# Optimization experiments

Hardware: AMD Instinct MI355X
Metric: run time of the kernel (lower is better)

The kernel has to match this reference:

```python
import jax, jax.numpy as jnp
import numpy as np

B, N = 1, 512
CS, CZ = 384, 128
H, DQK, DV, PQK, PV = 12, 16, 16, 4, 8
EPS = 1e-8
SW = float(np.sqrt(1.0 / (3 * DQK)))            # scalar_weights
PW = float(np.sqrt(1.0 / (3 * PQK * 9.0 / 2)))  # point_weights
ZW = float(np.sqrt(1.0 / 3))                    # attention_2d_weights


def _lin(key, din, dout):
    return 0.02 * jax.random.normal(key, (din, dout), dtype=jnp.float32), jnp.zeros((dout,), dtype=jnp.float32)


def setup_inputs():
    key = jax.random.key(0)
    ks = jax.random.split(key, 16)
    Wsq, bsq = _lin(ks[0], CS, H * DQK)
    Wsk, bsk = _lin(ks[1], CS, H * DQK)
    Wsv, bsv = _lin(ks[2], CS, H * DV)
    Wsb, bsb = _lin(ks[3], CZ, H)
    Wpq, bpq = _lin(ks[4], CS, H * PQK * 3)
    Wpk, bpk = _lin(ks[5], CS, H * PQK * 3)
    Wpv, bpv = _lin(ks[6], CS, H * PV * 3)
    Wout, bout = _lin(ks[7], H * (DV + PV * 4 + CZ), CS)
    w_attn = 0.5 * jax.random.normal(ks[8], (3,), dtype=jnp.float32)  # attn_linear weight (1,3)
    b_attn = jnp.zeros((), dtype=jnp.float32)
    tpw = jnp.full((H,), float(np.log(np.e - 1.0)), dtype=jnp.float32)  # trainable_point_weight
    s = jax.random.normal(ks[9], (B, N, CS), dtype=jnp.float32)
    z = jax.random.normal(ks[10], (B, N, N, CZ), dtype=jnp.float32)
    rot = jax.random.normal(ks[11], (B, N, 3, 3), dtype=jnp.float32)
    tran = jax.random.normal(ks[12], (B, N, 3), dtype=jnp.float32)
    res_mask = jnp.ones((B, N), dtype=jnp.float32)
    return dict(s=s, z=z, rot=rot, tran=tran, res_mask=res_mask,
                Wsq=Wsq, bsq=bsq, Wsk=Wsk, bsk=bsk, Wsv=Wsv, bsv=bsv,
                Wsb=Wsb, bsb=bsb, Wpq=Wpq, bpq=bpq, Wpk=Wpk, bpk=bpk,
                Wpv=Wpv, bpv=bpv, w_attn=w_attn, b_attn=b_attn, tpw=tpw,
                Wout=Wout, bout=bout)


def _ipa(s, z, rot, tran, res_mask, Wsq, bsq, Wsk, bsk, Wsv, bsv, Wsb, bsb,
         Wpq, bpq, Wpk, bpk, Wpv, bpv, w_attn, b_attn, tpw, Wout, bout):
    b, n, _ = s.shape
    sq = (s @ Wsq + bsq).reshape(b, n, H, DQK)
    sk = (s @ Wsk + bsk).reshape(b, n, H, DQK)
    sv = (s @ Wsv + bsv).reshape(b, n, H, DV)
    sb = z @ Wsb + bsb  # [b, i, j, h] pair bias

    def to_global(W, bias, p):
        t = (s @ W + bias).reshape(b, n, H, p, 3)
        return jnp.einsum('bnxy,bnhpy->bnhpx', rot, t) + tran[:, :, None, None, :]

    pqg = to_global(Wpq, bpq, PQK)
    pkg = to_global(Wpk, bpk, PQK)
    pvg = to_global(Wpv, bpv, PV)

    diff = pqg[:, :, None] - pkg[:, None, :]          # [b, i, j, h, p, 3]
    sdist = jnp.sum(diff * diff, axis=(-1, -2))       # [b, i, j, h]

    attn_point = -0.5 * jax.nn.softplus(tpw) * sdist * PW
    attn_scalar = jnp.einsum('bihd,bjhd->bijh', sq * SW, sk)
    attn_pair = sb * ZW
    # attn_linear(stack([scalar, point, pair], -1)).squeeze(-1)
    logits = attn_scalar * w_attn[0] + attn_point * w_attn[1] + attn_pair * w_attn[2] + b_attn

    mask2d = res_mask[:, :, None] * res_mask[:, None, :]
    logits = jnp.where(mask2d[..., None] == 0, jnp.finfo(logits.dtype).min, logits)
    attn = jax.nn.softmax(logits, axis=2)             # softmax over j

    r_scalar = jnp.einsum('bijh,bjhd->bihd', attn, sv)
    r_pt_g = jnp.einsum('bijh,bjhpc->bihpc', attn, pvg)
    # rotate back to local frame: R^T (x - t)
    r_pt = jnp.einsum('biyx,bihpy->bihpx', rot, r_pt_g - tran[:, :, None, None, :])
    r_norm = jnp.sqrt(jnp.sum(r_pt * r_pt, axis=-1) + EPS)  # [b, i, h, p]
    r_pair = jnp.einsum('bijh,bijc->bihc', attn, z)

    cat = jnp.concatenate([r_scalar, r_pt.reshape(b, n, H, PV * 3), r_norm, r_pair], axis=-1)
    return cat.reshape(b, n, -1) @ Wout + bout


def reference(s, z, rot, tran, res_mask, Wsq, bsq, Wsk, bsk, Wsv, bsv, Wsb, bsb,
              Wpq, bpq, Wpk, bpk, Wpv, bpv, w_attn, b_attn, tpw, Wout, bout):
    return _ipa(s, z, rot, tran, res_mask, Wsq, bsq, Wsk, bsk, Wsv, bsv, Wsb, bsb,
                Wpq, bpq, Wpk, bpk, Wpv, bpv, w_attn, b_attn, tpw, Wout, bout)
```

## Files before the change

kernel.cpp:

```cpp
#include <hip/hip_runtime.h>
#include <hip/hip_bf16.h>
#include <math.h>

#define NN 512
#define CSD 384
#define CZ 128
#define HH 12
#define TMPW 1152
#define CATH 176
#define CATDIM 2112
#define NSPLIT 6
#define KSPL 352

#define SW 0.14433756729740643f
#define PW 0.13608276348795434f
#define ZW 0.57735026918962576f
#define NEG_INF -3.4028234663852886e38f

typedef float f32x4_t __attribute__((ext_vector_type(4)));
typedef short bf16x8_t __attribute__((ext_vector_type(8)));

union BFU { uint4 q; bf16x8_t v; ushort u[8]; };

static __device__ __forceinline__ ushort f2bf(float f) {
    __hip_bfloat16 h = __float2bfloat16(f);
    return *reinterpret_cast<ushort*>(&h);
}
static __device__ __forceinline__ float bf2f(ushort u) {
    unsigned int v = ((unsigned int)u) << 16;
    return __uint_as_float(v);
}

__global__ void proj_gemm_kernel(const float* __restrict__ s,
                                 const float* __restrict__ Wsq, const float* __restrict__ bsq,
                                 const float* __restrict__ Wsk, const float* __restrict__ bsk,
                                 const float* __restrict__ Wsv, const float* __restrict__ bsv,
                                 const float* __restrict__ Wpq, const float* __restrict__ bpq,
                                 const float* __restrict__ Wpk, const float* __restrict__ bpk,
                                 const float* __restrict__ Wpv, const float* __restrict__ bpv,
                                 float* __restrict__ tmp)
{
    int bx = blockIdx.x;
    int n0 = blockIdx.y * 32;
    int f0 = bx * 48;
    const float* W; const float* bb; int dout; int segstart;
    if (bx < 4)       { W = Wsq; bb = bsq; dout = 192; segstart = 0; }
    else if (bx < 8)  { W = Wsk; bb = bsk; dout = 192; segstart = 192; }
    else if (bx < 12) { W = Wsv; bb = bsv; dout = 192; segstart = 384; }
    else if (bx < 15) { W = Wpq; bb = bpq; dout = 144; segstart = 576; }
    else if (bx < 18) { W = Wpk; bb = bpk; dout = 144; segstart = 720; }
    else              { W = Wpv; bb = bpv; dout = 288; segstart = 864; }
    int colbase = f0 - segstart;

    __shared__ float St[32][34];
    __shared__ float Ws[32][49];
    int tid = threadIdx.x;
    int ty = tid >> 4, tx = tid & 15;
    float acc[2][3] = {{0,0,0},{0,0,0}};

    for (int k0 = 0; k0 < CSD; k0 += 32) {
        {
            int r = tid >> 3, c4 = (tid & 7) * 4;
            float4 v = *(const float4*)&s[(size_t)(n0 + r) * CSD + k0 + c4];
            St[c4 + 0][r] = v.x; St[c4 + 1][r] = v.y; St[c4 + 2][r] = v.z; St[c4 + 3][r] = v.w;
        }
        for (int e = tid; e < 1536; e += 256) {
            int r = e / 48, c = e % 48;
            Ws[r][c] = W[(size_t)(k0 + r) * dout + colbase + c];
        }
        __syncthreads();
        #pragma unroll
        for (int k = 0; k < 32; k++) {
            float2 a = *(const float2*)&St[k][ty * 2];
            float b0 = Ws[k][tx * 3], b1 = Ws[k][tx * 3 + 1], b2 = Ws[k][tx * 3 + 2];
            acc[0][0] += a.x * b0; acc[0][1] += a.x * b1; acc[0][2] += a.x * b2;
            acc[1][0] += a.y * b0; acc[1][1] += a.y * b1; acc[1][2] += a.y * b2;
        }
        __syncthreads();
    }
    float bv0 = bb[colbase + tx * 3], bv1 = bb[colbase + tx * 3 + 1], bv2 = bb[colbase + tx * 3 + 2];
    #pragma unroll
    for (int r = 0; r < 2; r++) {
        float* o = tmp + (size_t)(n0 + ty * 2 + r) * TMPW + f0 + tx * 3;
        o[0] = acc[r][0] + bv0; o[1] = acc[r][1] + bv1; o[2] = acc[r][2] + bv2;
    }
}

__global__ void rotate_kernel(const float* __restrict__ rot, const float* __restrict__ tran,
                              float* __restrict__ tmp)
{
    int pid = blockIdx.x * 256 + threadIdx.x;
    int n = pid / 192, q = pid % 192;
    float* p = tmp + (size_t)n * TMPW + 576 + q * 3;
    float v0 = p[0], v1 = p[1], v2 = p[2];
    const float* R = rot + n * 9;
    const float* T = tran + n * 3;
    p[0] = R[0] * v0 + R[1] * v1 + R[2] * v2 + T[0];
    p[1] = R[3] * v0 + R[4] * v1 + R[5] * v2 + T[1];
    p[2] = R[6] * v0 + R[7] * v1 + R[8] * v2 + T[2];
}

__global__ void pairbias_mfma_kernel(const float* __restrict__ z, const float* __restrict__ Wsb,
                                     const float* __restrict__ watt, float* __restrict__ sbz)
{
    int tid = threadIdx.x;
    int w = tid >> 6, lane = tid & 63;
    int l16 = lane & 15, lhi = lane >> 4;
    float A2 = watt[2] * ZW;

    BFU breg[4];
    #pragma unroll
    for (int kk = 0; kk < 4; kk++) {
        #pragma unroll
        for (int e = 0; e < 8; e++) {
            int k = kk * 32 + lhi * 8 + e;
            float v = (l16 < HH) ? Wsb[k * HH + l16] * A2 : 0.f;
            breg[kk].u[e] = f2bf(v);
        }
    }

    #pragma unroll
    for (int t = 0; t < 4; t++) {
        size_t r0 = (size_t)blockIdx.x * 256 + (size_t)(t * 4 + w) * 16;
        const float* zrow = z + (r0 + l16) * CZ;
        f32x4_t acc = {0.f, 0.f, 0.f, 0.f};
        #pragma unroll
        for (int kk = 0; kk < 4; kk++) {
            int k0 = kk * 32 + lhi * 8;
            float4 f0 = *(const float4*)&zrow[k0];
            float4 f1 = *(const float4*)&zrow[k0 + 4];
            BFU a;
            a.u[0] = f2bf(f0.x); a.u[1] = f2bf(f0.y); a.u[2] = f2bf(f0.z); a.u[3] = f2bf(f0.w);
            a.u[4] = f2bf(f1.x); a.u[5] = f2bf(f1.y); a.u[6] = f2bf(f1.z); a.u[7] = f2bf(f1.w);
            acc = __builtin_amdgcn_mfma_f32_16x16x32_bf16(a.v, breg[kk].v, acc, 0, 0, 0);
        }
        if (l16 < HH) {
            #pragma unroll
            for (int r = 0; r < 4; r++)
                sbz[(r0 + lhi * 4 + r) * HH + l16] = acc[r];
        }
    }
}

__global__ void logits_softmax_kernel(const float* __restrict__ sbz, const float* __restrict__ resm,
                                      const float* __restrict__ bsb,
                                      const float* __restrict__ watt, const float* __restrict__ batt,
                                      const float* __restrict__ tpw, const float* __restrict__ tmp,
                                      ushort* __restrict__ attn_bf)
{
    int i = blockIdx.x;
    __shared__ float lt[NN * 17];
    __shared__ float sqs[192];
    __shared__ float pqi[144];
    __shared__ float cpt[12];
    __shared__ float cb[12];
    int tid = threadIdx.x;
    float w0 = watt[0], w1 = watt[1], w2 = watt[2], ba = batt[0];
    float A2 = w2 * ZW;

    for (int k = tid; k < 192; k += 256) sqs[k] = tmp[(size_t)i * TMPW + k] * (SW * w0);
    if (tid < 144) pqi[tid] = tmp[(size_t)i * TMPW + 576 + tid];
    if (tid < 12) {
        cpt[tid] = -0.5f * log1pf(expf(tpw[tid])) * PW * w1;
        cb[tid]  = A2 * bsb[tid] + ba;
    }
    __syncthreads();

    int jg = tid >> 2, hg = tid & 3, h0 = hg * 3;
    float rmi = resm[i];
    const float* sbi = sbz + (size_t)i * NN * HH;

    #pragma unroll
    for (int rr = 0; rr < 8; rr++) {
        int j = jg + 64 * rr;
        float mj = rmi * resm[j];
        const float* sbr = &sbi[(size_t)j * HH + h0];
        float pb[3] = { sbr[0], sbr[1], sbr[2] };
        #pragma unroll
        for (int t = 0; t < 3; t++) {
            int h = h0 + t;
            const float4* skp = (const float4*)(tmp + (size_t)j * TMPW + 192 + h * 16);
            const float4* sqp = (const float4*)&sqs[h * 16];
            float d0 = 0.f;
            #pragma unroll
            for (int q = 0; q < 4; q++) {
                float4 kv = skp[q];
                float4 qv = sqp[q];
                d0 += qv.x * kv.x + qv.y * kv.y + qv.z * kv.z + qv.w * kv.w;
            }
            const float4* pkp = (const float4*)(tmp + (size_t)j * TMPW + 720 + h * 12);
            const float4* pqp = (const float4*)&pqi[h * 12];
            float sd = 0.f;
            #pragma unroll
            for (int q = 0; q < 3; q++) {
                float4 kv = pkp[q];
                float4 qv = pqp[q];
                float a = qv.x - kv.x, bb2 = qv.y - kv.y, cc = qv.z - kv.z, e = qv.w - kv.w;
                sd += a * a + bb2 * bb2 + cc * cc + e * e;
            }
            float lg = cb[h] + pb[t] + d0 + cpt[h] * sd;
            if (mj == 0.f) lg = NEG_INF;
            lt[j * 17 + h] = lg;
        }
    }
    __syncthreads();

    int wid = tid >> 6, lane = tid & 63;
    #pragma unroll
    for (int t = 0; t < 3; t++) {
        int h = wid * 3 + t;
        float v[8]; float m = -INFINITY;
        #pragma unroll
        for (int u = 0; u < 8; u++) { v[u] = lt[(lane + 64 * u) * 17 + h]; m = fmaxf(m, v[u]); }
        for (int off = 32; off; off >>= 1) m = fmaxf(m, __shfl_xor(m, off));
        float ssum = 0.f;
        #pragma unroll
        for (int u = 0; u < 8; u++) { v[u] = __expf(v[u] - m); ssum += v[u]; }
        for (int off = 32; off; off >>= 1) ssum += __shfl_xor(ssum, off);
        float inv = 1.f / ssum;
        ushort* ag = attn_bf + ((size_t)i * HH + h) * NN;
        #pragma unroll
        for (int u = 0; u < 8; u++) ag[lane + 64 * u] = f2bf(v[u] * inv);
    }
}

__global__ void rpair_mfma_kernel(const float* __restrict__ z, const ushort* __restrict__ attn_bf,
                                  float* __restrict__ cat)
{
    int i = blockIdx.x;
    __shared__ uint4 Pl[16 * 64];
    int tid = threadIdx.x;

    const ushort* ab = attn_bf + (size_t)i * HH * NN;
    #pragma unroll
    for (int u = 0; u < 4; u++) {
        int s2 = tid + 256 * u;
        int m = s2 >> 6, g = s2 & 63;
        uint4 val;
        if (m < HH) val = *(const uint4*)&ab[(size_t)m * NN + g * 8];
        else { val.x = 0; val.y = 0; val.z = 0; val.w = 0; }
        Pl[m * 64 + (g ^ (m & 7))] = val;
    }
    __syncthreads();

    int w = tid >> 6, lane = tid & 63;
    int l16 = lane & 15, lhi = lane >> 4;
    int c0a = (w * 2 + 0) * 16, c0b = (w * 2 + 1) * 16;
    f32x4_t acc0 = {0.f, 0.f, 0.f, 0.f};
    f32x4_t acc1 = {0.f, 0.f, 0.f, 0.f};

    for (int kk = 0; kk < 16; kk++) {
        int gidx = kk * 4 + lhi;
        BFU au;
        au.q = Pl[l16 * 64 + (gidx ^ (l16 & 7))];
        const float* zb = z + ((size_t)i * NN + kk * 32 + lhi * 8) * CZ;
        BFU b0, b1;
        #pragma unroll
        for (int e = 0; e < 8; e++) {
            b0.u[e] = f2bf(zb[(size_t)e * CZ + c0a + l16]);
            b1.u[e] = f2bf(zb[(size_t)e * CZ + c0b + l16]);
        }
        acc0 = __builtin_amdgcn_mfma_f32_16x16x32_bf16(au.v, b0.v, acc0, 0, 0, 0);
        acc1 = __builtin_amdgcn_mfma_f32_16x16x32_bf16(au.v, b1.v, acc1, 0, 0, 0);
    }

    #pragma unroll
    for (int r = 0; r < 4; r++) {
        int h = lhi * 4 + r;
        if (h < HH) {
            float* cp = cat + (size_t)i * CATDIM + h * CATH + 48;
            cp[c0a + l16] = acc0[r];
            cp[c0b + l16] = acc1[r];
        }
    }
}

__global__ void head_sum_kernel(const ushort* __restrict__ attn_bf, const float* __restrict__ tmp,
                                const float* __restrict__ rot, const float* __restrict__ tran,
                                float* __restrict__ cat)
{
    int i0 = blockIdx.x * 32;
    int h  = blockIdx.y;
    __shared__ float At[32][65];
    __shared__ float Sr[64][44];
    __shared__ float Rp[32][24];
    int tid = threadIdx.x;
    int il = tid & 31, fg = tid >> 5;
    float acc[5] = {0,0,0,0,0};

    for (int jc = 0; jc < NN; jc += 64) {
        {
            int r = tid >> 3, c8 = (tid & 7) * 8;
            const ushort* src = attn_bf + ((size_t)(i0 + r) * HH + h) * NN + jc + c8;
            BFU v; v.q = *(const uint4*)src;
            #pragma unroll
            for (int q = 0; q < 8; q++) At[r][c8 + q] = bf2f(v.u[q]);
        }
        {
            int jr = tid >> 2, d4 = (tid & 3) * 4;
            *(float4*)&Sr[jr][d4] = *(const float4*)&tmp[(size_t)(jc + jr) * TMPW + 384 + h * 16 + d4];
        }
        for (int e = tid; e < 384; e += 256) {
            int jr = e / 6, p4 = (e % 6) * 4;
            *(float4*)&Sr[jr][16 + p4] = *(const float4*)&tmp[(size_t)(jc + jr) * TMPW + 864 + h * 24 + p4];
        }
        __syncthreads();
        #pragma unroll 4
        for (int j = 0; j < 64; j++) {
            float a = At[il][j];
            #pragma unroll
            for (int q = 0; q < 5; q++) acc[q] += a * Sr[j][fg * 5 + q];
        }
        __syncthreads();
    }

    float* cbase = cat + (size_t)(i0 + il) * CATDIM + h * CATH;
    #pragma unroll
    for (int q = 0; q < 5; q++) {
        int f = fg * 5 + q;
        if (f < 16) cbase[f] = acc[q];
        else Rp[il][f - 16] = acc[q];
    }
    __syncthreads();

    {
        int il2 = tid >> 3, p = tid & 7;
        int i = i0 + il2;
        float gx = Rp[il2][p * 3 + 0] - tran[i * 3 + 0];
        float gy = Rp[il2][p * 3 + 1] - tran[i * 3 + 1];
        float gz = Rp[il2][p * 3 + 2] - tran[i * 3 + 2];
        const float* R = rot + i * 9;
        float lx = R[0] * gx + R[3] * gy + R[6] * gz;
        float ly = R[1] * gx + R[4] * gy + R[7] * gz;
        float lz = R[2] * gx + R[5] * gy + R[8] * gz;
        float nrm = sqrtf(lx * lx + ly * ly + lz * lz + 1e-8f);
        float* cp = cat + (size_t)i * CATDIM + h * CATH;
        cp[16 + p * 3 + 0] = lx; cp[16 + p * 3 + 1] = ly; cp[16 + p * 3 + 2] = lz;
        cp[40 + p] = nrm;
    }
}

__global__ void out_gemm_split_kernel(const float* __restrict__ cat, const float* __restrict__ Wout,
                                      float* __restrict__ part)
{
    int n0 = blockIdx.x * 64;
    int i0 = blockIdx.y * 64;
    int ks = blockIdx.z * KSPL;
    __shared__ float St[32][68];
    __shared__ float Bs[32][68];
    int tid = threadIdx.x;
    int ty = tid >> 4, tx = tid & 15;
    float acc[4][4] = {{0,0,0,0},{0,0,0,0},{0,0,0,0},{0,0,0,0}};

    for (int k0 = 0; k0 < KSPL; k0 += 32) {
        {
            int r = tid >> 2, c8 = (tid & 3) * 8;
            const float* src = cat + (size_t)(i0 + r) * CATDIM + ks + k0 + c8;
            float4 v0 = *(const float4*)src;
            float4 v1 = *(const float4*)(src + 4);
            St[c8+0][r]=v0.x; St[c8+1][r]=v0.y; St[c8+2][r]=v0.z; St[c8+3][r]=v0.w;
            St[c8+4][r]=v1.x; St[c8+5][r]=v1.y; St[c8+6][r]=v1.z; St[c8+7][r]=v1.w;
        }
        {
            int r = tid >> 3, c8 = (tid & 7) * 8;
            const float* src = Wout + (size_t)(ks + k0 + r) * CSD + n0 + c8;
            *(float4*)&Bs[r][c8]     = *(const float4*)src;
            *(float4*)&Bs[r][c8 + 4] = *(const float4*)(src + 4);
        }
        __syncthreads();
        #pragma unroll
        for (int k = 0; k < 32; k++) {
            float4 a = *(const float4*)&St[k][ty * 4];
            float4 b = *(const float4*)&Bs[k][tx * 4];
            float av[4] = {a.x, a.y, a.z, a.w};
            float bv[4] = {b.x, b.y, b.z, b.w};
            #pragma unroll
            for (int r = 0; r < 4; r++)
                #pragma unroll
                for (int c = 0; c < 4; c++) acc[r][c] += av[r] * bv[c];
        }
        __syncthreads();
    }
    #pragma unroll
    for (int r = 0; r < 4; r++) {
        float4 v = make_float4(acc[r][0], acc[r][1], acc[r][2], acc[r][3]);
        *(float4*)&part[((size_t)blockIdx.z * NN + i0 + ty * 4 + r) * CSD + n0 + tx * 4] = v;
    }
}

__global__ void reduce_out_kernel(const float* __restrict__ part, const float* __restrict__ bout,
                                  float* __restrict__ out)
{
    int v = blockIdx.x * 256 + threadIdx.x;
    int n4 = v % 96;
    float4 o = ((const float4*)bout)[n4];
    const float4* p4 = (const float4*)part;
    #pragma unroll
    for (int s = 0; s < NSPLIT; s++) {
        float4 t = p4[(size_t)s * 49152 + v];
        o.x += t.x; o.y += t.y; o.z += t.z; o.w += t.w;
    }
    ((float4*)out)[v] = o;
}

extern "C" void kernel_launch(void* const* d_in, const int* in_sizes, int n_in,
                              void* d_out, int out_size, void* d_ws, size_t ws_size,
                              hipStream_t stream) {
    const float* s    = (const float*)d_in[0];
    const float* z    = (const float*)d_in[1];
    const float* rot  = (const float*)d_in[2];
    const float* tran = (const float*)d_in[3];
    const float* resm = (const float*)d_in[4];
    const float* Wsq  = (const float*)d_in[5];  const float* bsq = (const float*)d_in[6];
    const float* Wsk  = (const float*)d_in[7];  const float* bsk = (const float*)d_in[8];
    const float* Wsv  = (const float*)d_in[9];  const float* bsv = (const float*)d_in[10];
    const float* Wsb  = (const float*)d_in[11]; const float* bsb = (const float*)d_in[12];
    const float* Wpq  = (const float*)d_in[13]; const float* bpq = (const float*)d_in[14];
    const float* Wpk  = (const float*)d_in[15]; const float* bpk = (const float*)d_in[16];
    const float* Wpv  = (const float*)d_in[17]; const float* bpv = (const float*)d_in[18];
    const float* watt = (const float*)d_in[19]; const float* batt = (const float*)d_in[20];
    const float* tpw  = (const float*)d_in[21];
    const float* Wout = (const float*)d_in[22]; const float* bout = (const float*)d_in[23];
    float* out = (float*)d_out;
    float* ws  = (float*)d_ws;

    float* tmp      = ws;
    ushort* attn_bf = (ushort*)(ws + 589824);
    float* sbz      = ws + 589824 + 1572864;
    float* cat      = sbz + 3145728;
    float* partO    = cat + 1081344;

    proj_gemm_kernel<<<dim3(24, 16), 256, 0, stream>>>(s, Wsq, bsq, Wsk, bsk, Wsv, bsv,
                                                       Wpq, bpq, Wpk, bpk, Wpv, bpv, tmp);
    rotate_kernel<<<384, 256, 0, stream>>>(rot, tran, tmp);
    pairbias_mfma_kernel<<<1024, 256, 0, stream>>>(z, Wsb, watt, sbz);
    logits_softmax_kernel<<<512, 256, 0, stream>>>(sbz, resm, bsb, watt, batt, tpw,
                                                   tmp, attn_bf);
    rpair_mfma_kernel<<<512, 256, 0, stream>>>(z, attn_bf, cat);
    head_sum_kernel<<<dim3(16, 12), 256, 0, stream>>>(attn_bf, tmp, rot, tran, cat);
    out_gemm_split_kernel<<<dim3(6, 8, NSPLIT), 256, 0, stream>>>(cat, Wout, partO);
    reduce_out_kernel<<<192, 256, 0, stream>>>(partO, bout, out);
}
```

Baseline: 190.0 us.

## Emit transposed bf16 z during pair-bias pass and fuse frame rotation into projection

The pair-bias kernel now stages each row block of z in shared memory. Besides computing the bias, it writes a transposed bf16 copy of z. The rpair kernel then reads that copy with contiguous 16-byte loads instead of strided fp32 gathers with per-element conversion. The point rotation into global frames moves into the projection GEMM epilogue, which removes a separate launch. The trade is extra global writes of a 64 MB-class bf16 buffer (z_t is N*N*CZ bf16, about 64 MB) in exchange for half-size, coalesced reads in rpair.

```diff
diff --git a/kernel.cpp b/kernel.cpp
--- a/kernel.cpp
+++ b/kernel.cpp
@@ -31,7 +31,8 @@
     return __uint_as_float(v);
 }
 
-__global__ void proj_gemm_kernel(const float* __restrict__ s,
+__global__ void proj_gemm_kernel(const float* __restrict__ s, const float* __restrict__ rot,
+                                 const float* __restrict__ tran,
                                  const float* __restrict__ Wsq, const float* __restrict__ bsq,
                                  const float* __restrict__ Wsk, const float* __restrict__ bsk,
                                  const float* __restrict__ Wsv, const float* __restrict__ bsv,
@@ -81,30 +82,32 @@
     float bv0 = bb[colbase + tx * 3], bv1 = bb[colbase + tx * 3 + 1], bv2 = bb[colbase + tx * 3 + 2];
     #pragma unroll
     for (int r = 0; r < 2; r++) {
-        float* o = tmp + (size_t)(n0 + ty * 2 + r) * TMPW + f0 + tx * 3;
-        o[0] = acc[r][0] + bv0; o[1] = acc[r][1] + bv1; o[2] = acc[r][2] + bv2;
-    }
-}
-
-__global__ void rotate_kernel(const float* __restrict__ rot, const float* __restrict__ tran,
-                              float* __restrict__ tmp)
-{
-    int pid = blockIdx.x * 256 + threadIdx.x;
-    int n = pid / 192, q = pid % 192;
-    float* p = tmp + (size_t)n * TMPW + 576 + q * 3;
-    float v0 = p[0], v1 = p[1], v2 = p[2];
-    const float* R = rot + n * 9;
-    const float* T = tran + n * 3;
-    p[0] = R[0] * v0 + R[1] * v1 + R[2] * v2 + T[0];
-    p[1] = R[3] * v0 + R[4] * v1 + R[5] * v2 + T[1];
-    p[2] = R[6] * v0 + R[7] * v1 + R[8] * v2 + T[2];
-}
-
-__global__ void pairbias_mfma_kernel(const float* __restrict__ z, const float* __restrict__ Wsb,
-                                     const float* __restrict__ watt, float* __restrict__ sbz)
-{
-    int tid = threadIdx.x;
-    int w = tid >> 6, lane = tid & 63;
+        int n = n0 + ty * 2 + r;
+        float v0 = acc[r][0] + bv0, v1 = acc[r][1] + bv1, v2 = acc[r][2] + bv2;
+        float* o = tmp + (size_t)n * TMPW + f0 + tx * 3;
+        if (bx >= 12) {
+            const float* R = rot + n * 9;
+            const float* T = tran + n * 3;
+            float g0 = R[0] * v0 + R[1] * v1 + R[2] * v2 + T[0];
+            float g1 = R[3] * v0 + R[4] * v1 + R[5] * v2 + T[1];
+            float g2 = R[6] * v0 + R[7] * v1 + R[8] * v2 + T[2];
+            o[0] = g0; o[1] = g1; o[2] = g2;
+        } else {
+            o[0] = v0; o[1] = v1; o[2] = v2;
+        }
+    }
+}
+
+__global__ __launch_bounds__(256) void pairbias_zt_kernel(const float* __restrict__ z,
+                                                          const float* __restrict__ Wsb,
+                                                          const float* __restrict__ watt,
+                                                          float* __restrict__ sbz,
+                                                          ushort* __restrict__ z_t)
+{
+    int i = blockIdx.x;
+    __shared__ float zlin[64 * 132];
+    int tid = threadIdx.x;
+    int lane = tid & 63, w = tid >> 6;
     int l16 = lane & 15, lhi = lane >> 4;
     float A2 = watt[2] * ZW;
 
@@ -119,26 +122,60 @@
         }
     }
 
-    #pragma unroll
-    for (int t = 0; t < 4; t++) {
-        size_t r0 = (size_t)blockIdx.x * 256 + (size_t)(t * 4 + w) * 16;
-        const float* zrow = z + (r0 + l16) * CZ;
-        f32x4_t acc = {0.f, 0.f, 0.f, 0.f};
-        #pragma unroll
-        for (int kk = 0; kk < 4; kk++) {
-            int k0 = kk * 32 + lhi * 8;
-            float4 f0 = *(const float4*)&zrow[k0];
-            float4 f1 = *(const float4*)&zrow[k0 + 4];
-            BFU a;
-            a.u[0] = f2bf(f0.x); a.u[1] = f2bf(f0.y); a.u[2] = f2bf(f0.z); a.u[3] = f2bf(f0.w);
-            a.u[4] = f2bf(f1.x); a.u[5] = f2bf(f1.y); a.u[6] = f2bf(f1.z); a.u[7] = f2bf(f1.w);
-            acc = __builtin_amdgcn_mfma_f32_16x16x32_bf16(a.v, breg[kk].v, acc, 0, 0, 0);
-        }
-        if (l16 < HH) {
-            #pragma unroll
-            for (int r = 0; r < 4; r++)
-                sbz[(r0 + lhi * 4 + r) * HH + l16] = acc[r];
-        }
+    const float* zi = z + (size_t)i * NN * CZ;
+    ushort* zti = z_t + (size_t)i * CZ * NN;
+
+    for (int jt = 0; jt < 8; jt++) {
+        int j0 = jt * 64;
+        {
+            int r8 = tid >> 3, cq = tid & 7;
+            #pragma unroll
+            for (int p = 0; p < 2; p++) {
+                int row = r8 + p * 32;
+                const float* src = zi + (size_t)(j0 + row) * CZ;
+                #pragma unroll
+                for (int q = 0; q < 4; q++) {
+                    int c4 = (cq + q * 8) * 4;
+                    *(float4*)&zlin[row * 132 + c4] = *(const float4*)&src[c4];
+                }
+            }
+        }
+        __syncthreads();
+
+        {
+            f32x4_t acc = {0.f, 0.f, 0.f, 0.f};
+            #pragma unroll
+            for (int kk = 0; kk < 4; kk++) {
+                int c0 = kk * 32 + lhi * 8;
+                float4 f0 = *(const float4*)&zlin[(w * 16 + l16) * 132 + c0];
+                float4 f1 = *(const float4*)&zlin[(w * 16 + l16) * 132 + c0 + 4];
+                BFU a;
+                a.u[0] = f2bf(f0.x); a.u[1] = f2bf(f0.y); a.u[2] = f2bf(f0.z); a.u[3] = f2bf(f0.w);
+                a.u[4] = f2bf(f1.x); a.u[5] = f2bf(f1.y); a.u[6] = f2bf(f1.z); a.u[7] = f2bf(f1.w);
+                acc = __builtin_amdgcn_mfma_f32_16x16x32_bf16(a.v, breg[kk].v, acc, 0, 0, 0);
+            }
+            if (l16 < HH) {
+                #pragma unroll
+                for (int r = 0; r < 4; r++)
+                    sbz[((size_t)i * NN + j0 + w * 16 + lhi * 4 + r) * HH + l16] = acc[r];
+            }
+        }
+
+        {
+            int cbase = tid >> 3, jg = tid & 7;
+            #pragma unroll
+            for (int t = 0; t < 4; t++) {
+                int c = cbase + t * 32;
+                BFU o;
+                #pragma unroll
+                for (int q = 0; q < 8; q++) {
+                    int e = (q + jg) & 7;
+                    o.u[e] = f2bf(zlin[(jg * 8 + e) * 132 + c]);
+                }
+                *(uint4*)&zti[(size_t)c * NN + j0 + jg * 8] = o.q;
+            }
+        }
+        __syncthreads();
     }
 }
 
@@ -224,8 +261,9 @@
     }
 }
 
-__global__ void rpair_mfma_kernel(const float* __restrict__ z, const ushort* __restrict__ attn_bf,
-                                  float* __restrict__ cat)
+__global__ __launch_bounds__(256) void rpair_kernel(const ushort* __restrict__ z_t,
+                                                    const ushort* __restrict__ attn_bf,
+                                                    float* __restrict__ cat)
 {
     int i = blockIdx.x;
     __shared__ uint4 Pl[16 * 64];
@@ -245,32 +283,27 @@
 
     int w = tid >> 6, lane = tid & 63;
     int l16 = lane & 15, lhi = lane >> 4;
-    int c0a = (w * 2 + 0) * 16, c0b = (w * 2 + 1) * 16;
+    int c0 = w * 32;
+    const ushort* zti = z_t + (size_t)i * CZ * NN;
     f32x4_t acc0 = {0.f, 0.f, 0.f, 0.f};
     f32x4_t acc1 = {0.f, 0.f, 0.f, 0.f};
 
+    #pragma unroll 4
     for (int kk = 0; kk < 16; kk++) {
-        int gidx = kk * 4 + lhi;
-        BFU au;
-        au.q = Pl[l16 * 64 + (gidx ^ (l16 & 7))];
-        const float* zb = z + ((size_t)i * NN + kk * 32 + lhi * 8) * CZ;
-        BFU b0, b1;
-        #pragma unroll
-        for (int e = 0; e < 8; e++) {
-            b0.u[e] = f2bf(zb[(size_t)e * CZ + c0a + l16]);
-            b1.u[e] = f2bf(zb[(size_t)e * CZ + c0b + l16]);
-        }
-        acc0 = __builtin_amdgcn_mfma_f32_16x16x32_bf16(au.v, b0.v, acc0, 0, 0, 0);
-        acc1 = __builtin_amdgcn_mfma_f32_16x16x32_bf16(au.v, b1.v, acc1, 0, 0, 0);
-    }
-
-    #pragma unroll
-    for (int r = 0; r < 4; r++) {
-        int h = lhi * 4 + r;
-        if (h < HH) {
-            float* cp = cat + (size_t)i * CATDIM + h * CATH + 48;
-            cp[c0a + l16] = acc0[r];
-            cp[c0b + l16] = acc1[r];
+        BFU b; b.q = Pl[l16 * 64 + ((kk * 4 + lhi) ^ (l16 & 7))];
+        BFU a0, a1;
+        a0.q = *(const uint4*)&zti[(size_t)(c0 + l16) * NN + kk * 32 + lhi * 8];
+        a1.q = *(const uint4*)&zti[(size_t)(c0 + 16 + l16) * NN + kk * 32 + lhi * 8];
+        acc0 = __builtin_amdgcn_mfma_f32_16x16x32_bf16(a0.v, b.v, acc0, 0, 0, 0);
+        acc1 = __builtin_amdgcn_mfma_f32_16x16x32_bf16(a1.v, b.v, acc1, 0, 0, 0);
+    }
+
+    if (l16 < HH) {
+        float* cp = cat + (size_t)i * CATDIM + l16 * CATH + 48;
+        #pragma unroll
+        for (int r = 0; r < 4; r++) {
+            cp[c0 + lhi * 4 + r]      = acc0[r];
+            cp[c0 + 16 + lhi * 4 + r] = acc1[r];
         }
     }
 }
@@ -424,19 +457,20 @@
     float* out = (float*)d_out;
     float* ws  = (float*)d_ws;
 
-    float* tmp      = ws;
+    float*  tmp     = ws;
     ushort* attn_bf = (ushort*)(ws + 589824);
-    float* sbz      = ws + 589824 + 1572864;
-    float* cat      = sbz + 3145728;
-    float* partO    = cat + 1081344;
-
-    proj_gemm_kernel<<<dim3(24, 16), 256, 0, stream>>>(s, Wsq, bsq, Wsk, bsk, Wsv, bsv,
+    float*  sbz     = ws + 589824 + 1572864;
+    ushort* z_t     = (ushort*)(ws + 5308416);
+    float*  cat     = ws + 22085632;
+    float*  partO   = ws + 23166976;
+
+    proj_gemm_kernel<<<dim3(24, 16), 256, 0, stream>>>(s, rot, tran,
+                                                       Wsq, bsq, Wsk, bsk, Wsv, bsv,
                                                        Wpq, bpq, Wpk, bpk, Wpv, bpv, tmp);
-    rotate_kernel<<<384, 256, 0, stream>>>(rot, tran, tmp);
-    pairbias_mfma_kernel<<<1024, 256, 0, stream>>>(z, Wsb, watt, sbz);
+    pairbias_zt_kernel<<<512, 256, 0, stream>>>(z, Wsb, watt, sbz, z_t);
     logits_softmax_kernel<<<512, 256, 0, stream>>>(sbz, resm, bsb, watt, batt, tpw,
                                                    tmp, attn_bf);
-    rpair_mfma_kernel<<<512, 256, 0, stream>>>(z, attn_bf, cat);
+    rpair_kernel<<<512, 256, 0, stream>>>(z_t, attn_bf, cat);
     head_sum_kernel<<<dim3(16, 12), 256, 0, stream>>>(attn_bf, tmp, rot, tran, cat);
     out_gemm_split_kernel<<<dim3(6, 8, NSPLIT), 256, 0, stream>>>(cat, Wout, partO);
     reduce_out_kernel<<<192, 256, 0, stream>>>(partO, bout, out);
```

Result: slower. 222.0 us (+16.8%).
